# Kernel optimization log

Hardware: AMD Instinct MI355X
Metric: run time of the kernel (lower is better)

Reference implementation:

```python
import jax, jax.numpy as jnp
import numpy as np

N_POI, EMBED, N_EDGES, N_LAYERS, N_HEADS = 50000, 128, 800000, 2, 4
B, L = 512, 64  # sessions, session length (equal-length sections)


def setup_inputs() -> dict:
    key = jax.random.key(0)
    ks = jax.random.split(key, 12)
    d = EMBED
    return {
        "poi_embeds": jax.random.normal(ks[0], (N_POI, d), jnp.float32),
        "dist_edges": jax.random.randint(ks[1], (2, N_EDGES), 0, N_POI),
        "dist_vec": jax.random.uniform(ks[2], (N_EDGES,), jnp.float32),
        "data_poi": jax.random.randint(ks[3], (B,), 0, N_POI),
        "data_x": jax.random.randint(ks[4], (B * L,), 0, N_POI),
        "lin_w": jax.random.normal(ks[5], (N_LAYERS, d, d), jnp.float32) / np.sqrt(d),
        "lin_b": jnp.zeros((N_LAYERS, d), jnp.float32),
        "in_proj_w": jax.random.normal(ks[6], (3 * d, d), jnp.float32) / np.sqrt(d),
        "in_proj_b": jnp.zeros((3 * d,), jnp.float32),
        "out_proj_w": jax.random.normal(ks[7], (d, d), jnp.float32) / np.sqrt(d),
        "out_proj_b": jnp.zeros((d,), jnp.float32),
    }


def reference(poi_embeds, dist_edges, dist_vec, data_poi, data_x,
              lin_w, lin_b, in_proj_w, in_proj_b, out_proj_w, out_proj_b):
    n_poi, d = poi_embeds.shape
    # --- edge augmentation done in GeoGraph.__init__: reversed edges + self loops ---
    loop = jnp.arange(n_poi)
    edges = jnp.concatenate([dist_edges, dist_edges[::-1], jnp.stack([loop, loop])], axis=1)
    dvec = jnp.concatenate([dist_vec, dist_vec, jnp.zeros((n_poi,), dist_vec.dtype)])
    src, dst = edges[0], edges[1]
    # degree of source nodes (torch_geometric.utils.degree on nodes1)
    deg = jnp.zeros((n_poi,), poi_embeds.dtype).at[src].add(1.0)
    w = jax.lax.rsqrt(deg[src] * deg[dst]) * jnp.exp(-dvec ** 2)  # [E]

    enc = poi_embeds
    for i in range(lin_w.shape[0]):
        h = enc @ lin_w[i].T + lin_b[i]                              # [N, d]
        msg = w[:, None] * h[dst]                                    # [E, d] gather
        agg = jax.ops.segment_sum(msg, src, num_segments=n_poi)      # [N, d] scatter
        agg = jnp.where(agg >= 0, agg, 0.01 * agg)                   # leaky_relu(0.01)
        enc = agg / jnp.maximum(jnp.linalg.norm(agg, axis=-1, keepdims=True), 1e-12)

    tar_embed = enc[data_poi]                                        # [B, d]
    seq = enc[data_x].reshape(B, L, d)                               # padded sessions

    # --- nn.MultiheadAttention (batch_first) ---
    hd = d // N_HEADS
    qkv = seq @ in_proj_w.T + in_proj_b                              # [B, L, 3d]
    q, k, v = jnp.split(qkv, 3, axis=-1)
    heads = lambda t: t.reshape(B, L, N_HEADS, hd).transpose(0, 2, 1, 3)
    q, k, v = heads(q), heads(k), heads(v)
    scores = jnp.einsum('bhqd,bhkd->bhqk', q, k) / np.sqrt(hd)
    attn = jax.nn.softmax(scores, axis=-1)
    o = jnp.einsum('bhqk,bhkd->bhqd', attn, v).transpose(0, 2, 1, 3).reshape(B, L, d)
    o = o @ out_proj_w.T + out_proj_b

    aggr_feat = o.mean(axis=1)                                       # mean over padded length
    return aggr_feat, tar_embed
```

## Files before the change

kernel.cpp:

```cpp
#include <hip/hip_runtime.h>
#include <hip/hip_fp16.h>

#define NPOI 50000
#define EMB 128
#define NEDGE 800000
#define EAUG (2 * NEDGE + NPOI)
#define BATCH 512
#define SEQL 64
#define NHEADS 4
#define HDIM 32
#define NB 196
#define P1_BLOCKS ((NEDGE + 2047) / 2048)
#define SLAB_CAP 10240
#define BUCKET_CAP 10240

typedef _Float16 half8 __attribute__((ext_vector_type(8)));
typedef _Float16 half4 __attribute__((ext_vector_type(4)));
typedef _Float16 half2t __attribute__((ext_vector_type(2)));
typedef float f32x4 __attribute__((ext_vector_type(4)));
typedef unsigned long long u64;

union HBits { _Float16 h; unsigned short u; };


#define N4_POI (NPOI * 128 / 4)
#define N4_LIN (2 * 128 * 128 / 4)
#define N4_INW (384 * 128 / 4)
#define CVT_TOT (N4_POI + N4_LIN + N4_INW + NB)

__global__ void cvt_all_kernel(const float* __restrict__ poi, const float* __restrict__ linw,
                               const float* __restrict__ inw,
                               _Float16* __restrict__ poi_h, _Float16* __restrict__ linw_h,
                               _Float16* __restrict__ inw_h, int* __restrict__ bcur) {
    int i = blockIdx.x * blockDim.x + threadIdx.x;
    const float* src; _Float16* dst; int j = i;
    if (i < N4_POI) { src = poi; dst = poi_h; }
    else if (i < N4_POI + N4_LIN) { j = i - N4_POI; src = linw; dst = linw_h; }
    else if (i < N4_POI + N4_LIN + N4_INW) { j = i - N4_POI - N4_LIN; src = inw; dst = inw_h; }
    else if (i < CVT_TOT) { int b = i - (N4_POI + N4_LIN + N4_INW); bcur[b] = b * SLAB_CAP; return; }
    else return;
    float4 v = ((const float4*)src)[j];
    half4 h = { (_Float16)v.x, (_Float16)v.y, (_Float16)v.z, (_Float16)v.w };
    ((half4*)dst)[j] = h;
}


__global__ __launch_bounds__(256) void partition_kernel(
    const int* __restrict__ e0, const int* __restrict__ e1,
    const float* __restrict__ dv, int* __restrict__ bcur,
    u64* __restrict__ staging)
{
    __shared__ u64 stg[4096];
    __shared__ int lh[NB], lbase[NB], gb[NB];
    __shared__ int sc[256];
    const int t = threadIdx.x;
    const int blockBase = blockIdx.x * 2048;
    for (int j = t; j < NB; j += 256) lh[j] = 0;
    __syncthreads();

    u64 vals[16];
    unsigned br[16];
#pragma unroll
    for (int i = 0; i < 8; ++i) {
        br[2 * i] = 0xFFFFFFFFu;
        br[2 * i + 1] = 0xFFFFFFFFu;
        int g = blockBase + i * 256 + t;
        if (g < NEDGE) {
            int s = e0[g], d = e1[g];
            unsigned db = __float_as_uint(dv[g]);
            vals[2 * i]     = ((u64)s << 48) | ((u64)d << 32) | db;
            vals[2 * i + 1] = ((u64)d << 48) | ((u64)s << 32) | db;
            int bs = s >> 8, bd = d >> 8;
            int rs = atomicAdd(&lh[bs], 1);
            int rd_ = atomicAdd(&lh[bd], 1);
            br[2 * i]     = ((unsigned)bs << 16) | (unsigned)rs;
            br[2 * i + 1] = ((unsigned)bd << 16) | (unsigned)rd_;
        }
    }
    __syncthreads();
    sc[t] = (t < NB) ? lh[t] : 0;
    __syncthreads();
    for (int o = 1; o < 256; o <<= 1) {
        int u = (t >= o) ? sc[t - o] : 0;
        __syncthreads();
        sc[t] += u;
        __syncthreads();
    }
    if (t < NB) {
        lbase[t] = sc[t] - lh[t];
        gb[t] = (lh[t] > 0) ? atomicAdd(&bcur[t], lh[t]) : 0;
    }
    __syncthreads();
#pragma unroll
    for (int i = 0; i < 16; ++i) {
        if (br[i] != 0xFFFFFFFFu) {
            int b = br[i] >> 16, r = br[i] & 0xFFFF;
            stg[lbase[b] + r] = vals[i];
        }
    }
    __syncthreads();
    const int total = sc[255];
    for (int j = t; j < total; j += 256) {
        u64 v = stg[j];
        int b = (int)(v >> 56);
        staging[(size_t)gb[b] + (unsigned)(j - lbase[b])] = v;
    }
}


__global__ __launch_bounds__(256) void hist_kernel(const u64* __restrict__ staging,
                                                   const int* __restrict__ bcur,
                                                   float* __restrict__ rd,
                                                   int* __restrict__ bsum) {
    __shared__ int cnt[256];
    __shared__ int red[256];
    const int b = blockIdx.x, t = threadIdx.x;
    cnt[t] = 0;
    __syncthreads();
    const int base = b * SLAB_CAP;
    const int n = bcur[b] - base;
    for (int j = t; j < n; j += 256)
        atomicAdd(&cnt[(int)(staging[base + j] >> 48) & 255], 1);
    __syncthreads();
    int node = b * 256 + t;
    int rowsz = 0;
    if (node < NPOI) {
        rowsz = cnt[t] + 1;
        rd[node] = rsqrtf((float)rowsz);
    }
    red[t] = rowsz;
    __syncthreads();
    for (int o = 128; o > 0; o >>= 1) {
        if (t < o) red[t] += red[t + o];
        __syncthreads();
    }
    if (t == 0) bsum[b] = red[0];
}


__global__ __launch_bounds__(256) void csr_sort_kernel(
    const u64* __restrict__ staging, const int* __restrict__ bcur,
    const int* __restrict__ bsum, const float* __restrict__ rd,
    int* __restrict__ offs, unsigned* __restrict__ ew)
{
    const int k = blockIdx.x;
    const int node0 = k * 256;
    __shared__ unsigned outb[BUCKET_CAP];
    __shared__ int cnt[256], base2[256];
    __shared__ float rdl[256];
    __shared__ int bb_sh;
    const int t = threadIdx.x;
    const int node = node0 + t;
    cnt[t] = 0;
    rdl[t] = (node < NPOI) ? rd[node] : 0.f;
    {
        int partial = 0;
        for (int j = t; j < k; j += 256) partial += bsum[j];
        base2[t] = partial;
        __syncthreads();
        for (int o = 128; o > 0; o >>= 1) {
            if (t < o) base2[t] += base2[t + o];
            __syncthreads();
        }
        if (t == 0) bb_sh = base2[0];
        __syncthreads();
    }
    const int bucketbase = bb_sh;
    __syncthreads();
    const int sb = k * SLAB_CAP;
    const int n = bcur[k] - sb;
    for (int j = t; j < n; j += 256)
        atomicAdd(&cnt[(int)(staging[sb + j] >> 48) & 255], 1);
    __syncthreads();
    int rowsz = (node < NPOI) ? cnt[t] + 1 : 0;
    base2[t] = rowsz;
    __syncthreads();
    for (int o = 1; o < 256; o <<= 1) {
        int u = (t >= o) ? base2[t - o] : 0;
        __syncthreads();
        base2[t] += u;
        __syncthreads();
    }
    int myexc = base2[t] - rowsz;
    __syncthreads();
    base2[t] = myexc;
    cnt[t] = 0;
    if (node < NPOI) {
        offs[node] = bucketbase + myexc;
        if (node == NPOI - 1) offs[NPOI] = bucketbase + myexc + rowsz;
    }
    __syncthreads();
    for (int j = t; j < n; j += 256) {
        u64 e = staging[sb + j];
        int sl = (int)(e >> 48) & 255;
        int d = (int)(e >> 32) & 0xFFFF;
        float dist = __uint_as_float((unsigned)e);
        float w = rdl[sl] * rd[d] * expf(-dist * dist);
        HBits cv; cv.h = (_Float16)w;
        int r = atomicAdd(&cnt[sl], 1);
        outb[base2[sl] + r] = ((unsigned)d << 16) | cv.u;
    }
    __syncthreads();
    if (node < NPOI) {
        float w = rdl[t] * rdl[t];
        HBits cv; cv.h = (_Float16)w;
        outb[base2[t] + cnt[t]] = ((unsigned)node << 16) | cv.u;
    }
    __syncthreads();
    const int ntot = (node0 + 256 < NPOI ? n + 256 : n + (NPOI - node0));
    for (int j = t; j < ntot; j += 256) ew[bucketbase + j] = outb[j];
}


__global__ __launch_bounds__(256) void gemm_mfma_f16(
    const _Float16* __restrict__ A, const int* __restrict__ gidx,
    const _Float16* __restrict__ B, const float* __restrict__ bias,
    _Float16* __restrict__ C, int M, int N)
{
    __shared__ _Float16 Asl[64][136];
    __shared__ _Float16 Bsl[64][136];
    const int tid = threadIdx.x;
    const int n0 = blockIdx.x * 64;
    const int m0 = blockIdx.y * 64;

#pragma unroll
    for (int i = 0; i < 4; ++i) {
        int u = i * 256 + tid;
        int r = u >> 4;
        int c = u & 15;
        int row = m0 + r;
        int ar = (row < M) ? (gidx ? gidx[row] : row) : 0;
        *(float4*)&Asl[r][c * 8] = *(const float4*)(A + (size_t)ar * 128 + c * 8);
        *(float4*)&Bsl[r][c * 8] = *(const float4*)(B + (size_t)(n0 + r) * 128 + c * 8);
    }
    __syncthreads();

    const int wave = tid >> 6;
    const int lane = tid & 63;
    const int l15 = lane & 15;
    const int quad = lane >> 4;

    f32x4 acc[4];
#pragma unroll
    for (int mt = 0; mt < 4; ++mt) acc[mt] = (f32x4){0.f, 0.f, 0.f, 0.f};

#pragma unroll
    for (int ks = 0; ks < 4; ++ks) {
        half8 bfrag = *(const half8*)&Bsl[wave * 16 + l15][quad * 8 + ks * 32];
#pragma unroll
        for (int mt = 0; mt < 4; ++mt) {
            half8 afrag = *(const half8*)&Asl[mt * 16 + l15][quad * 8 + ks * 32];
            acc[mt] = __builtin_amdgcn_mfma_f32_16x16x32_f16(afrag, bfrag, acc[mt], 0, 0, 0);
        }
    }

    const int col = wave * 16 + l15;
    const float bv = bias[n0 + col];
    __syncthreads();
#pragma unroll
    for (int mt = 0; mt < 4; ++mt)
#pragma unroll
        for (int r = 0; r < 4; ++r)
            Asl[mt * 16 + quad * 4 + r][col] = (_Float16)(acc[mt][r] + bv);
    __syncthreads();
#pragma unroll
    for (int i = 0; i < 2; ++i) {
        int u = i * 256 + tid;
        int r = u >> 3;
        int c = u & 7;
        int m = m0 + r;
        if (m < M)
            *(half8*)(C + (size_t)m * N + n0 + c * 8) = *(const half8*)&Asl[r][c * 8];
    }
}


__global__ __launch_bounds__(64) void aggregate_kernel(
    const _Float16* __restrict__ h, const int* __restrict__ offs,
    const unsigned* __restrict__ ew, _Float16* __restrict__ enc_h)
{
    const int row = blockIdx.x;
    const int lane = threadIdx.x;
    const int beg = offs[row];
    const int end = offs[row + 1];
    float ax = 0.f, ay = 0.f;
#pragma unroll 8
    for (int e = beg; e < end; ++e) {
        unsigned p = ew[e];
        HBits cv; cv.u = (unsigned short)(p & 0xffffu);
        float w = (float)cv.h;
        int d = p >> 16;
        half2t hv = *(const half2t*)(h + (size_t)d * 128 + lane * 2);
        ax += w * (float)hv[0];
        ay += w * (float)hv[1];
    }
    ax = ax >= 0.f ? ax : 0.01f * ax;
    ay = ay >= 0.f ? ay : 0.01f * ay;
    float ss = ax * ax + ay * ay;
#pragma unroll
    for (int o = 32; o > 0; o >>= 1) ss += __shfl_xor(ss, o);
    float inv = 1.f / fmaxf(sqrtf(ss), 1e-12f);
    half2t hv = { (_Float16)(ax * inv), (_Float16)(ay * inv) };
    *(half2t*)(enc_h + (size_t)row * 128 + lane * 2) = hv;
}


__global__ __launch_bounds__(256) void attn_mfma_kernel(
    const _Float16* __restrict__ qkv, const float* __restrict__ outw,
    const float* __restrict__ outb, const _Float16* __restrict__ enc_h,
    const int* __restrict__ data_poi, float* __restrict__ out)
{
    const int b = blockIdx.x;
    const int wave = threadIdx.x >> 6;
    const int lane = threadIdx.x & 63;
    const int l15 = lane & 15;
    const int quad = lane >> 4;
    __shared__ _Float16 pP[NHEADS][64][72];
    __shared__ _Float16 vT[NHEADS][32][72];
    __shared__ float ob[128];
    const _Float16* base = qkv + (size_t)b * SEQL * 384;

    {
        const _Float16* vrow = base + (size_t)lane * 384 + 256 + wave * 32;
        half8 v0 = *(const half8*)(vrow);
        half8 v1 = *(const half8*)(vrow + 8);
        half8 v2 = *(const half8*)(vrow + 16);
        half8 v3 = *(const half8*)(vrow + 24);
#pragma unroll
        for (int j = 0; j < 8; ++j) {
            vT[wave][j][lane]      = v0[j];
            vT[wave][j + 8][lane]  = v1[j];
            vT[wave][j + 16][lane] = v2[j];
            vT[wave][j + 24][lane] = v3[j];
        }
    }

    half8 qf[4], kf[4];
#pragma unroll
    for (int t = 0; t < 4; ++t) {
        qf[t] = *(const half8*)(base + (size_t)(t * 16 + l15) * 384 + wave * 32 + quad * 8);
        kf[t] = *(const half8*)(base + (size_t)(t * 16 + l15) * 384 + 128 + wave * 32 + quad * 8);
    }

    f32x4 S[4][4];
#pragma unroll
    for (int lt = 0; lt < 4; ++lt)
#pragma unroll
        for (int mt = 0; mt < 4; ++mt) S[lt][mt] = (f32x4){0.f, 0.f, 0.f, 0.f};
#pragma unroll
    for (int lt = 0; lt < 4; ++lt)
#pragma unroll
        for (int mt = 0; mt < 4; ++mt)
            S[lt][mt] = __builtin_amdgcn_mfma_f32_16x16x32_f16(qf[lt], kf[mt], S[lt][mt], 0, 0, 0);

    const float scale = 0.17677669529663687f;
#pragma unroll
    for (int lt = 0; lt < 4; ++lt) {
#pragma unroll
        for (int r = 0; r < 4; ++r) {
            float m0 = -1e30f;
#pragma unroll
            for (int mt = 0; mt < 4; ++mt) {
                S[lt][mt][r] *= scale;
                m0 = fmaxf(m0, S[lt][mt][r]);
            }
#pragma unroll
            for (int o = 1; o < 16; o <<= 1) m0 = fmaxf(m0, __shfl_xor(m0, o));
            float s0 = 0.f;
#pragma unroll
            for (int mt = 0; mt < 4; ++mt) {
                float p = __expf(S[lt][mt][r] - m0);
                S[lt][mt][r] = p;
                s0 += p;
            }
#pragma unroll
            for (int o = 1; o < 16; o <<= 1) s0 += __shfl_xor(s0, o);
            float inv = 1.f / s0;
#pragma unroll
            for (int mt = 0; mt < 4; ++mt)
                pP[wave][lt * 16 + quad * 4 + r][mt * 16 + l15] = (_Float16)(S[lt][mt][r] * inv);
        }
    }
    __syncthreads();

    f32x4 O[4][2];
#pragma unroll
    for (int lt = 0; lt < 4; ++lt)
#pragma unroll
        for (int jt = 0; jt < 2; ++jt) O[lt][jt] = (f32x4){0.f, 0.f, 0.f, 0.f};
#pragma unroll
    for (int kh = 0; kh < 2; ++kh) {
        half8 vf[2];
#pragma unroll
        for (int jt = 0; jt < 2; ++jt)
            vf[jt] = *(const half8*)&vT[wave][jt * 16 + l15][kh * 32 + quad * 8];
#pragma unroll
        for (int lt = 0; lt < 4; ++lt) {
            half8 pf = *(const half8*)&pP[wave][lt * 16 + l15][kh * 32 + quad * 8];
#pragma unroll
            for (int jt = 0; jt < 2; ++jt)
                O[lt][jt] = __builtin_amdgcn_mfma_f32_16x16x32_f16(pf, vf[jt], O[lt][jt], 0, 0, 0);
        }
    }

#pragma unroll
    for (int jt = 0; jt < 2; ++jt) {
        float part = 0.f;
#pragma unroll
        for (int lt = 0; lt < 4; ++lt)
#pragma unroll
            for (int r = 0; r < 4; ++r) part += O[lt][jt][r];
        part += __shfl_xor(part, 16);
        part += __shfl_xor(part, 32);
        if (quad == 0) ob[wave * 32 + jt * 16 + l15] = part * (1.f / 64.f);
    }
    __syncthreads();

    int t = threadIdx.x;
    if (t < 128) {
        float val = outb[t];
        const float* wrow = outw + (size_t)t * 128;
#pragma unroll 8
        for (int k4 = 0; k4 < 32; ++k4) {
            float4 wv = *(const float4*)(wrow + k4 * 4);
            val += wv.x * ob[k4 * 4] + wv.y * ob[k4 * 4 + 1]
                 + wv.z * ob[k4 * 4 + 2] + wv.w * ob[k4 * 4 + 3];
        }
        out[(size_t)b * 128 + t] = val;
    } else {
        int j = t - 128;
        out[(size_t)(BATCH + b) * 128 + j] = (float)enc_h[(size_t)data_poi[b] * 128 + j];
    }
}


extern "C" void kernel_launch(void* const* d_in, const int* in_sizes, int n_in,
                              void* d_out, int out_size, void* d_ws, size_t ws_size,
                              hipStream_t stream)
{
    const float* poi      = (const float*)d_in[0];
    const int*   edges    = (const int*)d_in[1];
    const float* dvec     = (const float*)d_in[2];
    const int*   data_poi = (const int*)d_in[3];
    const int*   data_x   = (const int*)d_in[4];
    const float* lin_w    = (const float*)d_in[5];
    const float* lin_b    = (const float*)d_in[6];
    const float* inw      = (const float*)d_in[7];
    const float* inb      = (const float*)d_in[8];
    const float* outw     = (const float*)d_in[9];
    const float* outb     = (const float*)d_in[10];
    const int* e0 = edges;
    const int* e1 = edges + NEDGE;

    char* ws = (char*)d_ws;
    size_t off = 0;
    auto alloc = [&](size_t bytes) -> void* {
        void* p = ws + off;
        off = (off + bytes + 255) & ~(size_t)255;
        return p;
    };
    int*      offs   = (int*)     alloc((NPOI + 1) * 4);
    int*      bsum   = (int*)     alloc(NB * 4);
    int*      bcur   = (int*)     alloc(NB * 4);
    float*    rd     = (float*)   alloc(NPOI * 4);
    unsigned* ew     = (unsigned*)alloc((size_t)EAUG * 4);
    _Float16* enc_h  = (_Float16*)alloc((size_t)NPOI * 128 * 2);
    _Float16* linw_h = (_Float16*)alloc((size_t)2 * 128 * 128 * 2);
    _Float16* inw_h  = (_Float16*)alloc((size_t)384 * 128 * 2);
    char*     big    = (char*)    alloc(50ull * 1024 * 1024);
    _Float16* poi_h   = (_Float16*)big;
    u64*      staging = (u64*)(big + 16ull * 1024 * 1024);
    _Float16* hbuf    = (_Float16*)(big + 33ull * 1024 * 1024);
    _Float16* qkv_h   = (_Float16*)big;

    cvt_all_kernel<<<(CVT_TOT + 255) / 256, 256, 0, stream>>>(
        poi, lin_w, inw, poi_h, linw_h, inw_h, bcur);

    partition_kernel<<<P1_BLOCKS, 256, 0, stream>>>(e0, e1, dvec, bcur, staging);
    hist_kernel<<<NB, 256, 0, stream>>>(staging, bcur, rd, bsum);
    csr_sort_kernel<<<NB, 256, 0, stream>>>(staging, bcur, bsum, rd, offs, ew);

    gemm_mfma_f16<<<dim3(2, (NPOI + 63) / 64), 256, 0, stream>>>(
        poi_h, nullptr, linw_h, lin_b, hbuf, NPOI, 128);
    aggregate_kernel<<<NPOI, 64, 0, stream>>>(hbuf, offs, ew, enc_h);
    gemm_mfma_f16<<<dim3(2, (NPOI + 63) / 64), 256, 0, stream>>>(
        enc_h, nullptr, linw_h + 128 * 128, lin_b + 128, hbuf, NPOI, 128);
    aggregate_kernel<<<NPOI, 64, 0, stream>>>(hbuf, offs, ew, enc_h);

    gemm_mfma_f16<<<dim3(6, BATCH * SEQL / 64), 256, 0, stream>>>(
        enc_h, data_x, inw_h, inb, qkv_h, BATCH * SEQL, 384);
    attn_mfma_kernel<<<BATCH, 256, 0, stream>>>(qkv_h, outw, outb, enc_h, data_poi,
                                                (float*)d_out);
}
```

Baseline: 281.2 us.

## Fold degree normalization into GEMM epilogue, merge hist into CSR sort, widen aggregation

```diff
diff --git a/kernel.cpp b/kernel.cpp
--- a/kernel.cpp
+++ b/kernel.cpp
@@ -108,40 +108,9 @@
 }
 
 
-__global__ __launch_bounds__(256) void hist_kernel(const u64* __restrict__ staging,
-                                                   const int* __restrict__ bcur,
-                                                   float* __restrict__ rd,
-                                                   int* __restrict__ bsum) {
-    __shared__ int cnt[256];
-    __shared__ int red[256];
-    const int b = blockIdx.x, t = threadIdx.x;
-    cnt[t] = 0;
-    __syncthreads();
-    const int base = b * SLAB_CAP;
-    const int n = bcur[b] - base;
-    for (int j = t; j < n; j += 256)
-        atomicAdd(&cnt[(int)(staging[base + j] >> 48) & 255], 1);
-    __syncthreads();
-    int node = b * 256 + t;
-    int rowsz = 0;
-    if (node < NPOI) {
-        rowsz = cnt[t] + 1;
-        rd[node] = rsqrtf((float)rowsz);
-    }
-    red[t] = rowsz;
-    __syncthreads();
-    for (int o = 128; o > 0; o >>= 1) {
-        if (t < o) red[t] += red[t + o];
-        __syncthreads();
-    }
-    if (t == 0) bsum[b] = red[0];
-}
-
-
 __global__ __launch_bounds__(256) void csr_sort_kernel(
     const u64* __restrict__ staging, const int* __restrict__ bcur,
-    const int* __restrict__ bsum, const float* __restrict__ rd,
-    int* __restrict__ offs, unsigned* __restrict__ ew)
+    float* __restrict__ rd, int* __restrict__ offs, unsigned* __restrict__ ew)
 {
     const int k = blockIdx.x;
     const int node0 = k * 256;
@@ -151,11 +120,9 @@
     __shared__ int bb_sh;
     const int t = threadIdx.x;
     const int node = node0 + t;
-    cnt[t] = 0;
-    rdl[t] = (node < NPOI) ? rd[node] : 0.f;
     {
         int partial = 0;
-        for (int j = t; j < k; j += 256) partial += bsum[j];
+        for (int j = t; j < k; j += 256) partial += (bcur[j] - j * SLAB_CAP) + 256;
         base2[t] = partial;
         __syncthreads();
         for (int o = 128; o > 0; o >>= 1) {
@@ -166,6 +133,8 @@
         __syncthreads();
     }
     const int bucketbase = bb_sh;
+    __syncthreads();
+    cnt[t] = 0;
     __syncthreads();
     const int sb = k * SLAB_CAP;
     const int n = bcur[k] - sb;
@@ -173,6 +142,11 @@
         atomicAdd(&cnt[(int)(staging[sb + j] >> 48) & 255], 1);
     __syncthreads();
     int rowsz = (node < NPOI) ? cnt[t] + 1 : 0;
+    if (node < NPOI) {
+        float r_ = rsqrtf((float)rowsz);
+        rd[node] = r_;
+        rdl[t] = r_;
+    } else rdl[t] = 0.f;
     base2[t] = rowsz;
     __syncthreads();
     for (int o = 1; o < 256; o <<= 1) {
@@ -195,19 +169,18 @@
         int sl = (int)(e >> 48) & 255;
         int d = (int)(e >> 32) & 0xFFFF;
         float dist = __uint_as_float((unsigned)e);
-        float w = rdl[sl] * rd[d] * expf(-dist * dist);
+        float w = rdl[sl] * expf(-dist * dist);
         HBits cv; cv.h = (_Float16)w;
         int r = atomicAdd(&cnt[sl], 1);
         outb[base2[sl] + r] = ((unsigned)d << 16) | cv.u;
     }
     __syncthreads();
     if (node < NPOI) {
-        float w = rdl[t] * rdl[t];
-        HBits cv; cv.h = (_Float16)w;
+        HBits cv; cv.h = (_Float16)rdl[t];
         outb[base2[t] + cnt[t]] = ((unsigned)node << 16) | cv.u;
     }
     __syncthreads();
-    const int ntot = (node0 + 256 < NPOI ? n + 256 : n + (NPOI - node0));
+    const int ntot = n + ((node0 + 256 <= NPOI) ? 256 : (NPOI - node0));
     for (int j = t; j < ntot; j += 256) ew[bucketbase + j] = outb[j];
 }
 
@@ -215,6 +188,7 @@
 __global__ __launch_bounds__(256) void gemm_mfma_f16(
     const _Float16* __restrict__ A, const int* __restrict__ gidx,
     const _Float16* __restrict__ B, const float* __restrict__ bias,
+    const float* __restrict__ rs,
     _Float16* __restrict__ C, int M, int N)
 {
     __shared__ _Float16 Asl[64][136];
@@ -260,8 +234,12 @@
 #pragma unroll
     for (int mt = 0; mt < 4; ++mt)
 #pragma unroll
-        for (int r = 0; r < 4; ++r)
-            Asl[mt * 16 + quad * 4 + r][col] = (_Float16)(acc[mt][r] + bv);
+        for (int r = 0; r < 4; ++r) {
+            int m = m0 + mt * 16 + quad * 4 + r;
+            float v = acc[mt][r] + bv;
+            if (rs) { int mm = (m < M) ? m : 0; v *= rs[mm]; }
+            Asl[mt * 16 + quad * 4 + r][col] = (_Float16)v;
+        }
     __syncthreads();
 #pragma unroll
     for (int i = 0; i < 2; ++i) {
@@ -275,33 +253,48 @@
 }
 
 
-__global__ __launch_bounds__(64) void aggregate_kernel(
+__global__ __launch_bounds__(128) void aggregate_kernel(
     const _Float16* __restrict__ h, const int* __restrict__ offs,
     const unsigned* __restrict__ ew, _Float16* __restrict__ enc_h)
 {
-    const int row = blockIdx.x;
-    const int lane = threadIdx.x;
+    const int row = blockIdx.x * 2 + (threadIdx.x >> 6);
+    const int lane = threadIdx.x & 63;
+    const int e4 = lane >> 4;
+    const int c8 = lane & 15;
     const int beg = offs[row];
     const int end = offs[row + 1];
-    float ax = 0.f, ay = 0.f;
-#pragma unroll 8
-    for (int e = beg; e < end; ++e) {
-        unsigned p = ew[e];
+    float acc[8];
+#pragma unroll
+    for (int j = 0; j < 8; ++j) acc[j] = 0.f;
+#pragma unroll 2
+    for (int e = beg; e < end; e += 4) {
+        int idx = e + e4;
+        unsigned p = (idx < end) ? ew[idx] : 0u;
         HBits cv; cv.u = (unsigned short)(p & 0xffffu);
         float w = (float)cv.h;
         int d = p >> 16;
-        half2t hv = *(const half2t*)(h + (size_t)d * 128 + lane * 2);
-        ax += w * (float)hv[0];
-        ay += w * (float)hv[1];
-    }
-    ax = ax >= 0.f ? ax : 0.01f * ax;
-    ay = ay >= 0.f ? ay : 0.01f * ay;
-    float ss = ax * ax + ay * ay;
-#pragma unroll
-    for (int o = 32; o > 0; o >>= 1) ss += __shfl_xor(ss, o);
+        half8 hv = *(const half8*)(h + (size_t)d * 128 + c8 * 8);
+#pragma unroll
+        for (int j = 0; j < 8; ++j) acc[j] += w * (float)hv[j];
+    }
+#pragma unroll
+    for (int j = 0; j < 8; ++j) {
+        acc[j] += __shfl_xor(acc[j], 16);
+        acc[j] += __shfl_xor(acc[j], 32);
+        acc[j] = acc[j] >= 0.f ? acc[j] : 0.01f * acc[j];
+    }
+    float ss = 0.f;
+#pragma unroll
+    for (int j = 0; j < 8; ++j) ss += acc[j] * acc[j];
+#pragma unroll
+    for (int o = 1; o < 16; o <<= 1) ss += __shfl_xor(ss, o);
     float inv = 1.f / fmaxf(sqrtf(ss), 1e-12f);
-    half2t hv = { (_Float16)(ax * inv), (_Float16)(ay * inv) };
-    *(half2t*)(enc_h + (size_t)row * 128 + lane * 2) = hv;
+    if (e4 == 0) {
+        half8 hv;
+#pragma unroll
+        for (int j = 0; j < 8; ++j) hv[j] = (_Float16)(acc[j] * inv);
+        *(half8*)(enc_h + (size_t)row * 128 + c8 * 8) = hv;
+    }
 }
 
 
@@ -460,7 +453,6 @@
         return p;
     };
     int*      offs   = (int*)     alloc((NPOI + 1) * 4);
-    int*      bsum   = (int*)     alloc(NB * 4);
     int*      bcur   = (int*)     alloc(NB * 4);
     float*    rd     = (float*)   alloc(NPOI * 4);
     unsigned* ew     = (unsigned*)alloc((size_t)EAUG * 4);
@@ -477,18 +469,17 @@
         poi, lin_w, inw, poi_h, linw_h, inw_h, bcur);
 
     partition_kernel<<<P1_BLOCKS, 256, 0, stream>>>(e0, e1, dvec, bcur, staging);
-    hist_kernel<<<NB, 256, 0, stream>>>(staging, bcur, rd, bsum);
-    csr_sort_kernel<<<NB, 256, 0, stream>>>(staging, bcur, bsum, rd, offs, ew);
+    csr_sort_kernel<<<NB, 256, 0, stream>>>(staging, bcur, rd, offs, ew);
 
     gemm_mfma_f16<<<dim3(2, (NPOI + 63) / 64), 256, 0, stream>>>(
-        poi_h, nullptr, linw_h, lin_b, hbuf, NPOI, 128);
-    aggregate_kernel<<<NPOI, 64, 0, stream>>>(hbuf, offs, ew, enc_h);
+        poi_h, nullptr, linw_h, lin_b, rd, hbuf, NPOI, 128);
+    aggregate_kernel<<<NPOI / 2, 128, 0, stream>>>(hbuf, offs, ew, enc_h);
     gemm_mfma_f16<<<dim3(2, (NPOI + 63) / 64), 256, 0, stream>>>(
-        enc_h, nullptr, linw_h + 128 * 128, lin_b + 128, hbuf, NPOI, 128);
-    aggregate_kernel<<<NPOI, 64, 0, stream>>>(hbuf, offs, ew, enc_h);
+        enc_h, nullptr, linw_h + 128 * 128, lin_b + 128, rd, hbuf, NPOI, 128);
+    aggregate_kernel<<<NPOI / 2, 128, 0, stream>>>(hbuf, offs, ew, enc_h);
 
     gemm_mfma_f16<<<dim3(6, BATCH * SEQL / 64), 256, 0, stream>>>(
-        enc_h, data_x, inw_h, inb, qkv_h, BATCH * SEQL, 384);
+        enc_h, data_x, inw_h, inb, nullptr, qkv_h, BATCH * SEQL, 384);
     attn_mfma_kernel<<<BATCH, 256, 0, stream>>>(qkv_h, outw, outb, enc_h, data_poi,
                                                 (float*)d_out);
 }
```

Result: slower. 292.7 us (+4.1%).
